# Optimization experiments

Hardware: AMD Instinct MI355X
Metric: run time of the kernel (lower is better)

## Reference

```python
import jax, jax.numpy as jnp
import numpy as np

D_MODEL, N_STATE, E_INNER, K_CONV, DT_RANK = 1024, 16, 2048, 4, 64
EPS = 1e-6

def _silu(x):
    return x * jax.nn.sigmoid(x)

def _rmsnorm(x, w):
    var = jnp.mean(x * x, axis=-1, keepdims=True)
    return x * jax.lax.rsqrt(var + EPS) * w

def _causal_dwconv(x, conv_w):
    # x: [B, L, E]; conv_w: [E, 1, K] depthwise kernel
    xc = jnp.swapaxes(x, 1, 2)  # [B, E, L]
    xc = jnp.pad(xc, ((0, 0), (0, 0), (K_CONV - 1, 0)))
    y = jax.lax.conv_general_dilated(
        xc, conv_w, window_strides=(1,), padding='VALID',
        dimension_numbers=('NCL', 'OIL', 'NCL'), feature_group_count=E_INNER)
    return jnp.swapaxes(y, 1, 2)  # [B, L, E]

def _selective_scan(u, delta, A, Bm, Cm, Dp):
    # u, delta: [B, L, E]; Bm, Cm: [B, L, N]; A: [E, N]; Dp: [E]
    def step(h, inp):
        d_t, B_t, C_t, u_t = inp  # [B,E], [B,N], [B,N], [B,E]
        dA = jnp.exp(d_t[..., None] * A)                       # [B,E,N]
        h = dA * h + (d_t * u_t)[..., None] * B_t[:, None, :]  # [B,E,N]
        y = jnp.einsum('ben,bn->be', h, C_t)
        return h, y
    h0 = jnp.zeros((u.shape[0], E_INNER, N_STATE), u.dtype)
    xs = (jnp.swapaxes(delta, 0, 1), jnp.swapaxes(Bm, 0, 1),
          jnp.swapaxes(Cm, 0, 1), jnp.swapaxes(u, 0, 1))
    h_last, ys = jax.lax.scan(step, h0, xs)
    return jnp.swapaxes(ys, 0, 1) + u * Dp, h_last

def setup_inputs() -> dict:
    key = jax.random.key(0)
    ks = jax.random.split(key, 8)
    B, L = 4, 1024
    hidden_states = jax.random.normal(ks[0], (B, L, D_MODEL), jnp.float32)
    norm_w = jnp.ones((D_MODEL,), jnp.float32)
    W_in = jax.random.normal(ks[1], (D_MODEL, 2 * E_INNER), jnp.float32) * (D_MODEL ** -0.5)
    conv_w = jax.random.normal(ks[2], (E_INNER, 1, K_CONV), jnp.float32) * (K_CONV ** -0.5)
    W_x = jax.random.normal(ks[3], (E_INNER, DT_RANK + 2 * N_STATE), jnp.float32) * (E_INNER ** -0.5)
    W_dt = jax.random.normal(ks[4], (DT_RANK, E_INNER), jnp.float32) * (DT_RANK ** -0.5)
    # dt bias so softplus(b) lands roughly in [delta_min, delta_max]
    dt = jnp.exp(jax.random.uniform(ks[5], (E_INNER,)) * (np.log(0.1) - np.log(0.001)) + np.log(0.001))
    b_dt = dt + jnp.log(-jnp.expm1(-dt))  # inverse softplus
    A_log = jnp.log(jnp.broadcast_to(jnp.arange(1, N_STATE + 1, dtype=jnp.float32), (E_INNER, N_STATE)))
    D_param = jnp.ones((E_INNER,), jnp.float32)
    W_out = jax.random.normal(ks[6], (E_INNER, D_MODEL), jnp.float32) * (E_INNER ** -0.5)
    return {"hidden_states": hidden_states, "norm_w": norm_w, "W_in": W_in,
            "conv_w": conv_w, "W_x": W_x, "W_dt": W_dt, "b_dt": b_dt,
            "A_log": A_log, "D_param": D_param, "W_out": W_out}

def reference(hidden_states, norm_w, W_in, conv_w, W_x, W_dt, b_dt, A_log, D_param, W_out):
    residual = hidden_states
    x = _rmsnorm(hidden_states, norm_w)
    xz = jnp.einsum('bld,de->ble', x, W_in)          # [B,L,2E]
    x_in, z = jnp.split(xz, 2, axis=-1)
    x_act = _silu(_causal_dwconv(x_in, conv_w))      # [B,L,E]
    x_db = jnp.einsum('ble,er->blr', x_act, W_x)     # [B,L,R+2N]
    dt_lr = x_db[..., :DT_RANK]
    Bm = x_db[..., DT_RANK:DT_RANK + N_STATE]
    Cm = x_db[..., DT_RANK + N_STATE:]
    delta = jax.nn.softplus(jnp.einsum('blr,re->ble', dt_lr, W_dt) + b_dt)
    A = -jnp.exp(A_log)
    y, h_last = _selective_scan(x_act, delta, A, Bm, Cm, D_param)
    y = y * _silu(z)
    out = jnp.einsum('ble,ed->bld', y, W_out)
    # dropout is identity in eval mode
    return residual + out, h_last
```

## Files before the change

kernel.cpp:

```cpp
#include <hip/hip_runtime.h>
#include <cstdint>
#include <cstddef>

#define DM 1024
#define EI 2048
#define NS 16
#define DR 64
#define BB 4
#define LL 1024
#define MM (BB*LL)
#define NCHUNK 32
#define CHUNK 32

typedef __attribute__((ext_vector_type(8))) __bf16 bf16x8;
typedef __attribute__((ext_vector_type(4))) float f32x4;
typedef __attribute__((ext_vector_type(8))) unsigned short u16x8;

__device__ __forceinline__ unsigned short f2bf(float f) {
    union { float f; unsigned int u; } v; v.f = f;
    unsigned int r = v.u + 0x7FFFu + ((v.u >> 16) & 1u);
    return (unsigned short)(r >> 16);
}
__device__ __forceinline__ float bf2f(unsigned short u) {
    union { unsigned int u; float f; } v; v.u = ((unsigned int)u) << 16;
    return v.f;
}

__device__ __forceinline__ void gload_lds16(const unsigned short* g, unsigned short* l) {
    __builtin_amdgcn_global_load_lds(
        (const __attribute__((address_space(1))) unsigned int*)g,
        (__attribute__((address_space(3))) unsigned int*)l, 16, 0, 0);
}

__global__ void rmsnorm_bf16(const float* __restrict__ x, const float* __restrict__ w,
                             unsigned short* __restrict__ out) {
    int m = blockIdx.x, tid = threadIdx.x;
    const float4* row = (const float4*)(x + (size_t)m * DM);
    float4 v = row[tid];
    float ss = v.x*v.x + v.y*v.y + v.z*v.z + v.w*v.w;
    #pragma unroll
    for (int o = 32; o; o >>= 1) ss += __shfl_down(ss, o);
    __shared__ float red[4];
    if ((tid & 63) == 0) red[tid >> 6] = ss;
    __syncthreads();
    ss = red[0] + red[1] + red[2] + red[3];
    float scale = rsqrtf(ss * (1.0f / DM) + 1e-6f);
    const float4* wr = (const float4*)w;
    float4 wv = wr[tid];
    ushort4 o4;
    o4.x = f2bf(v.x * scale * wv.x);
    o4.y = f2bf(v.y * scale * wv.y);
    o4.z = f2bf(v.z * scale * wv.z);
    o4.w = f2bf(v.w * scale * wv.w);
    ((ushort4*)out)[(size_t)m * (DM/4) + tid] = o4;
}

__global__ void transpose_all(const float* __restrict__ W_in, const float* __restrict__ W_x,
                              const float* __restrict__ W_dt, const float* __restrict__ W_out,
                              unsigned short* __restrict__ wt_in, unsigned short* __restrict__ wt_x,
                              unsigned short* __restrict__ wt_dt, unsigned short* __restrict__ wt_out) {
    __shared__ float t[32][33];
    int id = blockIdx.x;
    const float* in; unsigned short* out;
    int R, C, Cpad, bx, by;
    if (id < 4096)      { in = W_in;  out = wt_in;  R = 1024; C = 4096; Cpad = 4096; bx = id & 127; by = id >> 7; }
    else if (id < 4352) { id -= 4096; in = W_x;  out = wt_x;  R = 2048; C = 96;  Cpad = 128;  bx = id & 3;  by = id >> 2; }
    else if (id < 4480) { id -= 4352; in = W_dt; out = wt_dt; R = 64;   C = 2048; Cpad = 2048; bx = id & 63; by = id >> 6; }
    else                { id -= 4480; in = W_out; out = wt_out; R = 2048; C = 1024; Cpad = 1024; bx = id & 31; by = id >> 5; }
    int c0 = bx * 32, r0 = by * 32;
    int tx = threadIdx.x, ty = threadIdx.y;
    #pragma unroll
    for (int j = 0; j < 32; j += 8) {
        int r = r0 + ty + j, c = c0 + tx;
        t[ty + j][tx] = (r < R && c < C) ? in[(size_t)r * C + c] : 0.f;
    }
    __syncthreads();
    #pragma unroll
    for (int j = 0; j < 32; j += 8) {
        int c = c0 + ty + j, r = r0 + tx;
        if (c < Cpad && r < R) out[(size_t)c * R + r] = f2bf(t[tx][ty + j]);
    }
}

template<int EPI>
__global__ void gemm_mfma(const unsigned short* __restrict__ A,
                          const unsigned short* __restrict__ Bt,
                          float* __restrict__ C,
                          const float* __restrict__ ex1,
                          unsigned short* __restrict__ exb,
                          int M, int N, int K, int ldc) {
    __shared__ __attribute__((aligned(16))) unsigned short lds_a[128 * 32];
    __shared__ __attribute__((aligned(16))) unsigned short lds_b[128 * 32];
    const int tid = threadIdx.x;
    const int w = tid >> 6, lane = tid & 63;
    const int m0 = blockIdx.y * 128;
    const int n0 = (EPI == 3) ? 0 : blockIdx.x * 128;
    const int kstart = (EPI == 3) ? blockIdx.x * (K >> 3) : 0;
    const int kend   = (EPI == 3) ? kstart + (K >> 3) : K;
    const int wm = (w & 1) * 64, wn = (w >> 1) * 64;
    const int q = lane >> 4, r = lane & 15;
    const int srow = lane >> 2;
    const int scol = (lane & 3) * 8;

    f32x4 acc[4][4];
    f32x4 zero = {0.f, 0.f, 0.f, 0.f};
    #pragma unroll
    for (int i = 0; i < 4; ++i)
        #pragma unroll
        for (int j = 0; j < 4; ++j) acc[i][j] = zero;

    for (int kb = kstart; kb < kend; kb += 32) {
        __syncthreads();
        #pragma unroll
        for (int j = 0; j < 2; ++j) {
            int rbase = w * 32 + j * 16;
            gload_lds16(A  + (size_t)(m0 + rbase + srow) * K + kb + scol, lds_a + rbase * 32);
            gload_lds16(Bt + (size_t)(n0 + rbase + srow) * K + kb + scol, lds_b + rbase * 32);
        }
        __syncthreads();
        bf16x8 af[4], bfr[4];
        #pragma unroll
        for (int mi = 0; mi < 4; ++mi)
            af[mi] = *(const bf16x8*)(lds_a + (wm + mi * 16 + r) * 32 + q * 8);
        #pragma unroll
        for (int ni = 0; ni < 4; ++ni)
            bfr[ni] = *(const bf16x8*)(lds_b + (wn + ni * 16 + r) * 32 + q * 8);
        #pragma unroll
        for (int mi = 0; mi < 4; ++mi)
            #pragma unroll
            for (int ni = 0; ni < 4; ++ni)
                acc[mi][ni] = __builtin_amdgcn_mfma_f32_16x16x32_bf16(af[mi], bfr[ni], acc[mi][ni], 0, 0, 0);
    }

    #pragma unroll
    for (int mi = 0; mi < 4; ++mi) {
        #pragma unroll
        for (int ni = 0; ni < 4; ++ni) {
            f32x4 v = acc[mi][ni];
            int gmb = m0 + wm + mi * 16 + q * 4;
            int gn  = n0 + wn + ni * 16 + r;
            #pragma unroll
            for (int t = 0; t < 4; ++t) {
                int gm = gmb + t;
                float val = v[t];
                if (EPI == 1) {
                    C[(size_t)gm * ldc + gn] = val + ex1[(size_t)gm * ldc + gn];
                } else if (EPI == 2) {
                    val += ex1[gn];
                    val = fmaxf(val, 0.f) + log1pf(__expf(-fabsf(val)));
                    exb[(size_t)gm * ldc + gn] = f2bf(val);
                } else if (EPI == 3) {
                    C[((size_t)blockIdx.x * M + gm) * 128 + gn] = val;
                } else {
                    exb[(size_t)gm * ldc + gn] = f2bf(val);
                }
            }
        }
    }
}

__global__ void xproj_reduce(const float* __restrict__ Pp,
                             unsigned short* __restrict__ dtlr, float* __restrict__ bc) {
    int id = blockIdx.x * 256 + threadIdx.x;
    int n = id & 127, m = id >> 7;
    if (n >= DR + 2 * NS) return;
    float s = 0.f;
    #pragma unroll
    for (int ks = 0; ks < 8; ++ks)
        s += Pp[((size_t)ks * MM + m) * 128 + n];
    if (n < DR) dtlr[(size_t)m * DR + n] = f2bf(s);
    else bc[(size_t)m * 32 + (n - DR)] = s;
}

__global__ void conv_silu8(const unsigned short* __restrict__ xzb, const float* __restrict__ cw,
                           unsigned short* __restrict__ xab) {
    size_t idx8 = ((size_t)blockIdx.x * 256 + threadIdx.x) * 8;
    int e = (int)(idx8 & (EI - 1));
    size_t m = idx8 >> 11;
    int l = (int)(m & (LL - 1));
    u16x8 x0 = *(const u16x8*)(xzb + m * 4096 + e);
    u16x8 zer = {0,0,0,0,0,0,0,0};
    u16x8 x1 = (l >= 1) ? *(const u16x8*)(xzb + (m - 1) * 4096 + e) : zer;
    u16x8 x2 = (l >= 2) ? *(const u16x8*)(xzb + (m - 2) * 4096 + e) : zer;
    u16x8 x3 = (l >= 3) ? *(const u16x8*)(xzb + (m - 3) * 4096 + e) : zer;
    u16x8 o;
    #pragma unroll
    for (int j = 0; j < 8; ++j) {
        float4 wv = ((const float4*)cw)[e + j];
        float s = bf2f(x0[j]) * wv.w + bf2f(x1[j]) * wv.z
                + bf2f(x2[j]) * wv.y + bf2f(x3[j]) * wv.x;
        float a = s / (1.f + __expf(-s));
        o[j] = f2bf(a);
    }
    *(u16x8*)(xab + idx8) = o;
}

__global__ void scan_phase1(const unsigned short* __restrict__ dbufb, const unsigned short* __restrict__ xu,
                            const float* __restrict__ bc, const float* __restrict__ A_log,
                            float* __restrict__ P, float* __restrict__ H) {
    int e = blockIdx.x * 256 + threadIdx.x;
    int c = blockIdx.y, b = blockIdx.z;
    float A[NS], h[NS], p[NS];
    #pragma unroll
    for (int n = 0; n < NS; ++n) {
        A[n] = -expf(A_log[(size_t)e * NS + n]);
        h[n] = 0.f; p[n] = 1.f;
    }
    int mbase = b * LL + c * CHUNK;
    for (int t = 0; t < CHUNK; ++t) {
        size_t m = (size_t)(mbase + t);
        float d = bf2f(dbufb[m * 2048 + e]);
        float u = bf2f(xu[m * 2048 + e]);
        float du = d * u;
        const float* Bv = bc + m * 32;
        #pragma unroll
        for (int n = 0; n < NS; ++n) {
            float dA = __expf(d * A[n]);
            p[n] *= dA;
            h[n] = fmaf(dA, h[n], du * Bv[n]);
        }
    }
    size_t base = ((size_t)(b * NCHUNK + c) * NS) * 2048 + e;
    #pragma unroll
    for (int n = 0; n < NS; ++n) {
        P[base + (size_t)n * 2048] = p[n];
        H[base + (size_t)n * 2048] = h[n];
    }
}

__global__ void scan_phase2(const float* __restrict__ P, const float* __restrict__ H,
                            float* __restrict__ h0, float* __restrict__ hlast) {
    int id = blockIdx.x * 256 + threadIdx.x;
    int e = id & (EI - 1);
    int bn = id >> 11;
    int n = bn & (NS - 1), b = bn >> 4;
    float h = 0.f;
    #pragma unroll
    for (int c = 0; c < NCHUNK; ++c) {
        size_t ix = (((size_t)(b * NCHUNK + c) * NS) + n) * 2048 + e;
        h0[ix] = h;
        h = fmaf(P[ix], h, H[ix]);
    }
    hlast[(((size_t)b * EI + e) * NS) + n] = h;
}

__global__ void scan_phase3(const unsigned short* __restrict__ dbufb, const unsigned short* __restrict__ xu,
                            const unsigned short* __restrict__ xzb,
                            const float* __restrict__ bc, const float* __restrict__ A_log,
                            const float* __restrict__ Dp, const float* __restrict__ h0,
                            unsigned short* __restrict__ ybf) {
    int e = blockIdx.x * 256 + threadIdx.x;
    int c = blockIdx.y, b = blockIdx.z;
    float A[NS], h[NS];
    size_t base = ((size_t)(b * NCHUNK + c) * NS) * 2048 + e;
    #pragma unroll
    for (int n = 0; n < NS; ++n) {
        A[n] = -expf(A_log[(size_t)e * NS + n]);
        h[n] = h0[base + (size_t)n * 2048];
    }
    float D = Dp[e];
    int mbase = b * LL + c * CHUNK;
    for (int t = 0; t < CHUNK; ++t) {
        size_t m = (size_t)(mbase + t);
        float d = bf2f(dbufb[m * 2048 + e]);
        float u = bf2f(xu[m * 2048 + e]);
        float du = d * u;
        const float* Bv = bc + m * 32;
        float y = 0.f;
        #pragma unroll
        for (int n = 0; n < NS; ++n) {
            float dA = __expf(d * A[n]);
            h[n] = fmaf(dA, h[n], du * Bv[n]);
            y = fmaf(h[n], Bv[16 + n], y);
        }
        y = fmaf(u, D, y);
        float z = bf2f(xzb[m * 4096 + 2048 + e]);
        float sil = z / (1.f + __expf(-z));
        ybf[m * 2048 + e] = f2bf(y * sil);
    }
}

extern "C" void kernel_launch(void* const* d_in, const int* in_sizes, int n_in,
                              void* d_out, int out_size, void* d_ws, size_t ws_size,
                              hipStream_t stream) {
    (void)in_sizes; (void)n_in; (void)out_size; (void)ws_size;
    const float* hidden = (const float*)d_in[0];
    const float* norm_w = (const float*)d_in[1];
    const float* W_in   = (const float*)d_in[2];
    const float* conv_w = (const float*)d_in[3];
    const float* W_x    = (const float*)d_in[4];
    const float* W_dt   = (const float*)d_in[5];
    const float* b_dt   = (const float*)d_in[6];
    const float* A_log  = (const float*)d_in[7];
    const float* D_par  = (const float*)d_in[8];
    const float* W_out  = (const float*)d_in[9];
    float* out = (float*)d_out;
    char* ws = (char*)d_ws;
    const size_t MB = 1ull << 20;

    unsigned short* xzb      = (unsigned short*)(ws + 0);
    unsigned short* xact_bf  = (unsigned short*)(ws + 32 * MB);
    unsigned short* xnorm_bf = (unsigned short*)(ws + 48 * MB);
    unsigned short* wt_in    = (unsigned short*)(ws + 56 * MB);
    unsigned short* wt_out   = (unsigned short*)(ws + 64 * MB);
    unsigned short* wt_x     = (unsigned short*)(ws + 68 * MB);
    unsigned short* wt_dt    = (unsigned short*)(ws + 68 * MB + 512 * 1024);
    unsigned short* dtlr     = (unsigned short*)(ws + 69 * MB);
    float*          bc       = (float*)(ws + 69 * MB + 512 * 1024);
    unsigned short* dbufb    = (unsigned short*)(ws + 70 * MB);
    unsigned short* ybf      = (unsigned short*)(ws + 86 * MB);
    float*          h0       = (float*)(ws + 102 * MB);
    float*          P        = (float*)(ws + 118 * MB);
    float*          Hb       = (float*)(ws + 134 * MB);
    float* Ppart = P;
    float* hlast = out + (size_t)MM * DM;

    rmsnorm_bf16<<<MM, 256, 0, stream>>>(hidden, norm_w, xnorm_bf);
    transpose_all<<<6528, dim3(32, 8), 0, stream>>>(W_in, W_x, W_dt, W_out,
                                                    wt_in, wt_x, wt_dt, wt_out);

    gemm_mfma<4><<<dim3(32, 32), 256, 0, stream>>>(xnorm_bf, wt_in, nullptr, nullptr, xzb,
                                                   MM, 4096, 1024, 4096);
    conv_silu8<<<(MM * EI) / (256 * 8), 256, 0, stream>>>(xzb, conv_w, xact_bf);
    gemm_mfma<3><<<dim3(8, 32), 256, 0, stream>>>(xact_bf, wt_x, Ppart, nullptr, nullptr,
                                                  MM, 128, 2048, 128);
    xproj_reduce<<<(MM * 128) / 256, 256, 0, stream>>>(Ppart, dtlr, bc);
    gemm_mfma<2><<<dim3(16, 32), 256, 0, stream>>>(dtlr, wt_dt, nullptr, b_dt, dbufb,
                                                   MM, 2048, 64, 2048);
    scan_phase1<<<dim3(8, NCHUNK, BB), 256, 0, stream>>>(dbufb, xact_bf, bc, A_log, P, Hb);
    scan_phase2<<<(BB * NS * EI) / 256, 256, 0, stream>>>(P, Hb, h0, hlast);
    scan_phase3<<<dim3(8, NCHUNK, BB), 256, 0, stream>>>(dbufb, xact_bf, xzb, bc, A_log, D_par, h0, ybf);
    gemm_mfma<1><<<dim3(8, 32), 256, 0, stream>>>(ybf, wt_out, out, hidden, nullptr,
                                                  MM, 1024, 2048, 1024);
}
```

Baseline: 331.7 us.

## Merge prologue kernels, fold scan carry into phase3, split-K out-projection

Merges the rmsnorm and weight-transpose kernels into one launch. Drops scan_phase2: each phase3 block now rebuilds its starting state by running the chunk carry over all earlier chunks itself, and the last chunk writes h_last. The out-projection GEMM becomes a 4-way split-K over 1024 blocks that writes bf16 partials, and a new reduce kernel sums them and adds the residual. This cuts launches and raises parallelism for the 256-block output GEMM. The cost is redundant carry work in phase3, which grows with the chunk index, and reduced precision from rounding the partials to bf16.

```diff
diff --git a/kernel.cpp b/kernel.cpp
--- a/kernel.cpp
+++ b/kernel.cpp
@@ -32,35 +32,36 @@
         (__attribute__((address_space(3))) unsigned int*)l, 16, 0, 0);
 }
 
-__global__ void rmsnorm_bf16(const float* __restrict__ x, const float* __restrict__ w,
-                             unsigned short* __restrict__ out) {
-    int m = blockIdx.x, tid = threadIdx.x;
-    const float4* row = (const float4*)(x + (size_t)m * DM);
-    float4 v = row[tid];
-    float ss = v.x*v.x + v.y*v.y + v.z*v.z + v.w*v.w;
-    #pragma unroll
-    for (int o = 32; o; o >>= 1) ss += __shfl_down(ss, o);
-    __shared__ float red[4];
-    if ((tid & 63) == 0) red[tid >> 6] = ss;
-    __syncthreads();
-    ss = red[0] + red[1] + red[2] + red[3];
-    float scale = rsqrtf(ss * (1.0f / DM) + 1e-6f);
-    const float4* wr = (const float4*)w;
-    float4 wv = wr[tid];
-    ushort4 o4;
-    o4.x = f2bf(v.x * scale * wv.x);
-    o4.y = f2bf(v.y * scale * wv.y);
-    o4.z = f2bf(v.z * scale * wv.z);
-    o4.w = f2bf(v.w * scale * wv.w);
-    ((ushort4*)out)[(size_t)m * (DM/4) + tid] = o4;
-}
-
-__global__ void transpose_all(const float* __restrict__ W_in, const float* __restrict__ W_x,
-                              const float* __restrict__ W_dt, const float* __restrict__ W_out,
-                              unsigned short* __restrict__ wt_in, unsigned short* __restrict__ wt_x,
-                              unsigned short* __restrict__ wt_dt, unsigned short* __restrict__ wt_out) {
+__global__ void pre_all(const float* __restrict__ W_in, const float* __restrict__ W_x,
+                        const float* __restrict__ W_dt, const float* __restrict__ W_out,
+                        const float* __restrict__ x, const float* __restrict__ nw,
+                        unsigned short* __restrict__ wt_in, unsigned short* __restrict__ wt_x,
+                        unsigned short* __restrict__ wt_dt, unsigned short* __restrict__ wt_out,
+                        unsigned short* __restrict__ xnorm) {
+    int id = blockIdx.x;
+    int tx = threadIdx.x, ty = threadIdx.y;
+    if (id >= 6528) {
+        int m = id - 6528, tid = ty * 32 + tx;
+        const float4* row = (const float4*)(x + (size_t)m * DM);
+        float4 v = row[tid];
+        float ss = v.x*v.x + v.y*v.y + v.z*v.z + v.w*v.w;
+        #pragma unroll
+        for (int o = 32; o; o >>= 1) ss += __shfl_down(ss, o);
+        __shared__ float red[4];
+        if ((tid & 63) == 0) red[tid >> 6] = ss;
+        __syncthreads();
+        ss = red[0] + red[1] + red[2] + red[3];
+        float scale = rsqrtf(ss * (1.0f / DM) + 1e-6f);
+        float4 wv = ((const float4*)nw)[tid];
+        ushort4 o4;
+        o4.x = f2bf(v.x * scale * wv.x);
+        o4.y = f2bf(v.y * scale * wv.y);
+        o4.z = f2bf(v.z * scale * wv.z);
+        o4.w = f2bf(v.w * scale * wv.w);
+        ((ushort4*)xnorm)[(size_t)m * (DM/4) + tid] = o4;
+        return;
+    }
     __shared__ float t[32][33];
-    int id = blockIdx.x;
     const float* in; unsigned short* out;
     int R, C, Cpad, bx, by;
     if (id < 4096)      { in = W_in;  out = wt_in;  R = 1024; C = 4096; Cpad = 4096; bx = id & 127; by = id >> 7; }
@@ -68,7 +69,6 @@
     else if (id < 4480) { id -= 4352; in = W_dt; out = wt_dt; R = 64;   C = 2048; Cpad = 2048; bx = id & 63; by = id >> 6; }
     else                { id -= 4480; in = W_out; out = wt_out; R = 2048; C = 1024; Cpad = 1024; bx = id & 31; by = id >> 5; }
     int c0 = bx * 32, r0 = by * 32;
-    int tx = threadIdx.x, ty = threadIdx.y;
     #pragma unroll
     for (int j = 0; j < 32; j += 8) {
         int r = r0 + ty + j, c = c0 + tx;
@@ -95,8 +95,10 @@
     const int w = tid >> 6, lane = tid & 63;
     const int m0 = blockIdx.y * 128;
     const int n0 = (EPI == 3) ? 0 : blockIdx.x * 128;
-    const int kstart = (EPI == 3) ? blockIdx.x * (K >> 3) : 0;
-    const int kend   = (EPI == 3) ? kstart + (K >> 3) : K;
+    const int kstart = (EPI == 3) ? blockIdx.x * (K >> 3)
+                     : (EPI == 5) ? blockIdx.z * (K >> 2) : 0;
+    const int kend   = (EPI == 3) ? kstart + (K >> 3)
+                     : (EPI == 5) ? kstart + (K >> 2) : K;
     const int wm = (w & 1) * 64, wn = (w >> 1) * 64;
     const int q = lane >> 4, r = lane & 15;
     const int srow = lane >> 2;
@@ -143,16 +145,16 @@
             for (int t = 0; t < 4; ++t) {
                 int gm = gmb + t;
                 float val = v[t];
-                if (EPI == 1) {
-                    C[(size_t)gm * ldc + gn] = val + ex1[(size_t)gm * ldc + gn];
-                } else if (EPI == 2) {
+                if (EPI == 2) {
                     val += ex1[gn];
                     val = fmaxf(val, 0.f) + log1pf(__expf(-fabsf(val)));
                     exb[(size_t)gm * ldc + gn] = f2bf(val);
                 } else if (EPI == 3) {
                     C[((size_t)blockIdx.x * M + gm) * 128 + gn] = val;
+                } else if (EPI == 4) {
+                    exb[(size_t)gm * ldc + gn] = f2bf(val);
                 } else {
-                    exb[(size_t)gm * ldc + gn] = f2bf(val);
+                    exb[((size_t)blockIdx.z * M + gm) * ldc + gn] = f2bf(val);
                 }
             }
         }
@@ -170,6 +172,20 @@
         s += Pp[((size_t)ks * MM + m) * 128 + n];
     if (n < DR) dtlr[(size_t)m * DR + n] = f2bf(s);
     else bc[(size_t)m * 32 + (n - DR)] = s;
+}
+
+__global__ void outproj_reduce(const unsigned short* __restrict__ Pp,
+                               const float* __restrict__ resid, float* __restrict__ out) {
+    int id = blockIdx.x * 256 + threadIdx.x;
+    int c4 = id & 255;
+    int m  = id >> 8;
+    float4 s = ((const float4*)(resid + (size_t)m * DM))[c4];
+    #pragma unroll
+    for (int z = 0; z < 4; ++z) {
+        ushort4 p = *(const ushort4*)(Pp + ((size_t)z * MM + m) * DM + c4 * 4);
+        s.x += bf2f(p.x); s.y += bf2f(p.y); s.z += bf2f(p.z); s.w += bf2f(p.w);
+    }
+    ((float4*)(out + (size_t)m * DM))[c4] = s;
 }
 
 __global__ void conv_silu8(const unsigned short* __restrict__ xzb, const float* __restrict__ cw,
@@ -228,35 +244,25 @@
     }
 }
 
-__global__ void scan_phase2(const float* __restrict__ P, const float* __restrict__ H,
-                            float* __restrict__ h0, float* __restrict__ hlast) {
-    int id = blockIdx.x * 256 + threadIdx.x;
-    int e = id & (EI - 1);
-    int bn = id >> 11;
-    int n = bn & (NS - 1), b = bn >> 4;
-    float h = 0.f;
-    #pragma unroll
-    for (int c = 0; c < NCHUNK; ++c) {
-        size_t ix = (((size_t)(b * NCHUNK + c) * NS) + n) * 2048 + e;
-        h0[ix] = h;
-        h = fmaf(P[ix], h, H[ix]);
-    }
-    hlast[(((size_t)b * EI + e) * NS) + n] = h;
-}
-
 __global__ void scan_phase3(const unsigned short* __restrict__ dbufb, const unsigned short* __restrict__ xu,
                             const unsigned short* __restrict__ xzb,
                             const float* __restrict__ bc, const float* __restrict__ A_log,
-                            const float* __restrict__ Dp, const float* __restrict__ h0,
-                            unsigned short* __restrict__ ybf) {
+                            const float* __restrict__ Dp,
+                            const float* __restrict__ P, const float* __restrict__ H,
+                            unsigned short* __restrict__ ybf, float* __restrict__ hlast) {
     int e = blockIdx.x * 256 + threadIdx.x;
     int c = blockIdx.y, b = blockIdx.z;
     float A[NS], h[NS];
-    size_t base = ((size_t)(b * NCHUNK + c) * NS) * 2048 + e;
     #pragma unroll
     for (int n = 0; n < NS; ++n) {
         A[n] = -expf(A_log[(size_t)e * NS + n]);
-        h[n] = h0[base + (size_t)n * 2048];
+        h[n] = 0.f;
+    }
+    for (int cc = 0; cc < c; ++cc) {
+        size_t base = ((size_t)(b * NCHUNK + cc) * NS) * 2048 + e;
+        #pragma unroll
+        for (int n = 0; n < NS; ++n)
+            h[n] = fmaf(P[base + (size_t)n * 2048], h[n], H[base + (size_t)n * 2048]);
     }
     float D = Dp[e];
     int mbase = b * LL + c * CHUNK;
@@ -277,6 +283,11 @@
         float z = bf2f(xzb[m * 4096 + 2048 + e]);
         float sil = z / (1.f + __expf(-z));
         ybf[m * 2048 + e] = f2bf(y * sil);
+    }
+    if (c == NCHUNK - 1) {
+        #pragma unroll
+        for (int n = 0; n < NS; ++n)
+            hlast[(((size_t)b * EI + e) * NS) + n] = h[n];
     }
 }
 
@@ -309,16 +320,14 @@
     float*          bc       = (float*)(ws + 69 * MB + 512 * 1024);
     unsigned short* dbufb    = (unsigned short*)(ws + 70 * MB);
     unsigned short* ybf      = (unsigned short*)(ws + 86 * MB);
-    float*          h0       = (float*)(ws + 102 * MB);
-    float*          P        = (float*)(ws + 118 * MB);
-    float*          Hb       = (float*)(ws + 134 * MB);
+    float*          P        = (float*)(ws + 102 * MB);
+    float*          Hb       = (float*)(ws + 118 * MB);
+    unsigned short* Pout     = (unsigned short*)(ws + 102 * MB);
     float* Ppart = P;
     float* hlast = out + (size_t)MM * DM;
 
-    rmsnorm_bf16<<<MM, 256, 0, stream>>>(hidden, norm_w, xnorm_bf);
-    transpose_all<<<6528, dim3(32, 8), 0, stream>>>(W_in, W_x, W_dt, W_out,
-                                                    wt_in, wt_x, wt_dt, wt_out);
-
+    pre_all<<<10624, dim3(32, 8), 0, stream>>>(W_in, W_x, W_dt, W_out, hidden, norm_w,
+                                               wt_in, wt_x, wt_dt, wt_out, xnorm_bf);
     gemm_mfma<4><<<dim3(32, 32), 256, 0, stream>>>(xnorm_bf, wt_in, nullptr, nullptr, xzb,
                                                    MM, 4096, 1024, 4096);
     conv_silu8<<<(MM * EI) / (256 * 8), 256, 0, stream>>>(xzb, conv_w, xact_bf);
@@ -328,8 +337,9 @@
     gemm_mfma<2><<<dim3(16, 32), 256, 0, stream>>>(dtlr, wt_dt, nullptr, b_dt, dbufb,
                                                    MM, 2048, 64, 2048);
     scan_phase1<<<dim3(8, NCHUNK, BB), 256, 0, stream>>>(dbufb, xact_bf, bc, A_log, P, Hb);
-    scan_phase2<<<(BB * NS * EI) / 256, 256, 0, stream>>>(P, Hb, h0, hlast);
-    scan_phase3<<<dim3(8, NCHUNK, BB), 256, 0, stream>>>(dbufb, xact_bf, xzb, bc, A_log, D_par, h0, ybf);
-    gemm_mfma<1><<<dim3(8, 32), 256, 0, stream>>>(ybf, wt_out, out, hidden, nullptr,
-                                                  MM, 1024, 2048, 1024);
-}
+    scan_phase3<<<dim3(8, NCHUNK, BB), 256, 0, stream>>>(dbufb, xact_bf, xzb, bc, A_log, D_par,
+                                                         P, Hb, ybf, hlast);
+    gemm_mfma<5><<<dim3(8, 32, 4), 256, 0, stream>>>(ybf, wt_out, nullptr, nullptr, Pout,
+                                                     MM, 1024, 2048, 1024);
+    outproj_reduce<<<(MM * DM / 4) / 256, 256, 0, stream>>>(Pout, hidden, out);
+}
```

New measurement: 393.5 us. 18.6% more time.
